# Kernel tuning notes

Measured on AMD Instinct MI355X. Metric: run time of the kernel, lower is better.

Reference implementation:

```python
import jax, jax.numpy as jnp
import numpy as np

N_HEADS = 16
ROPE_BASE = 10000.0


def _rope_tables(T, head_dim, dtype):
    inv_freq = 1.0 / (ROPE_BASE ** (jnp.arange(0, head_dim, 2, dtype=jnp.float32) / head_dim))
    t = jnp.arange(T, dtype=jnp.float32)
    freqs = jnp.outer(t, inv_freq)              # (T, head_dim/2)
    emb = jnp.concatenate([freqs, freqs], -1)   # (T, head_dim)
    return jnp.cos(emb).astype(dtype), jnp.sin(emb).astype(dtype)


def _rotate_half(x):
    x1, x2 = jnp.split(x, 2, axis=-1)
    return jnp.concatenate([-x2, x1], axis=-1)


def setup_inputs() -> dict:
    key = jax.random.key(0)
    k1, k2, k3 = jax.random.split(key, 3)
    B, T, C = 2, 2048, 2048
    x = jax.random.normal(k1, (B, T, C), dtype=jnp.float32)
    Wqkv = jax.random.normal(k2, (C, 3 * C), dtype=jnp.float32) * (1.0 / np.sqrt(C))
    Wproj = jax.random.normal(k3, (C, C), dtype=jnp.float32) * (1.0 / np.sqrt(C))
    return {"x": x, "Wqkv": Wqkv, "Wproj": Wproj}


def reference(x, Wqkv, Wproj):
    B, T, C = x.shape
    H = N_HEADS
    D = C // H
    qkv = jnp.einsum('btc,cd->btd', x, Wqkv)            # (B,T,3C)
    q, k, v = jnp.split(qkv, 3, axis=-1)
    # (B,T,C) -> (B,H,T,D)
    q = q.reshape(B, T, H, D).transpose(0, 2, 1, 3)
    k = k.reshape(B, T, H, D).transpose(0, 2, 1, 3)
    v = v.reshape(B, T, H, D).transpose(0, 2, 1, 3)
    cos, sin = _rope_tables(T, D, x.dtype)              # (T,D) each
    q = q * cos + _rotate_half(q) * sin
    k = k * cos + _rotate_half(k) * sin
    scale = 1.0 / jnp.sqrt(jnp.asarray(D, x.dtype))
    att = jnp.einsum('bhqd,bhkd->bhqk', q, k) * scale   # (B,H,T,T)
    causal = jnp.tril(jnp.ones((T, T), dtype=bool))
    att = jnp.where(causal, att, jnp.asarray(-jnp.inf, att.dtype))
    att = jax.nn.softmax(att, axis=-1)
    y = jnp.einsum('bhqk,bhkd->bhqd', att, v)           # (B,H,T,D)
    y = y.transpose(0, 2, 1, 3).reshape(B, T, C)
    return jnp.einsum('btc,cd->btd', y, Wproj)
```

## Files before the change

kernel.cpp:

```cpp
#include <hip/hip_runtime.h>
#include <stdint.h>

#define T_SEQ 2048
#define NH 16
#define HD 128
#define CC 2048
#define N3 6144
#define MM 4096

typedef short bf16x8 __attribute__((ext_vector_type(8)));
typedef float f32x4 __attribute__((ext_vector_type(4)));

__device__ __forceinline__ unsigned short f2bf(float f) {
  unsigned int u = __float_as_uint(f);
  u += 0x7FFF + ((u >> 16) & 1);
  return (unsigned short)(u >> 16);
}
__device__ __forceinline__ float bf2f(unsigned short h) {
  return __uint_as_float(((unsigned int)h) << 16);
}

__global__ __launch_bounds__(256) void k_transpose_cvt(const float* __restrict__ in,
                                                       unsigned short* __restrict__ out,
                                                       int K, int N) {
  __shared__ float tile[32][33];
  int k0 = blockIdx.x * 32;
  int n0 = blockIdx.y * 32;
  int tx = threadIdx.x & 31, ty = threadIdx.x >> 5;
  #pragma unroll
  for (int r = ty; r < 32; r += 8)
    tile[r][tx] = in[(size_t)(k0 + r) * N + n0 + tx];
  __syncthreads();
  #pragma unroll
  for (int r = ty; r < 32; r += 8)
    out[(size_t)(n0 + r) * K + k0 + tx] = f2bf(tile[tx][r]);
}

__global__ __launch_bounds__(256) void k_cvt(const float* __restrict__ in,
                                             unsigned short* __restrict__ out, int n4) {
  int i = blockIdx.x * 256 + threadIdx.x;
  if (i >= n4) return;
  float4 v = ((const float4*)in)[i];
  ushort4 o;
  o.x = f2bf(v.x); o.y = f2bf(v.y); o.z = f2bf(v.z); o.w = f2bf(v.w);
  ((ushort4*)out)[i] = o;
}

template<int NJ, int EPI, int MMAJ>
__global__ __launch_bounds__(512, 1) void k_gemm8(const unsigned short* __restrict__ A,
                                                  const unsigned short* __restrict__ Bt,
                                                  float* __restrict__ C,
                                                  unsigned short* __restrict__ qo,
                                                  unsigned short* __restrict__ ko,
                                                  unsigned short* __restrict__ vo,
                                                  int M, int N, int K) {
  constexpr int BU = NJ / 2;
  constexpr int DSTRIDE = (1 + BU) * 16384;
  extern __shared__ __align__(16) char lds[];
  const int tid = threadIdx.x;
  const int lane = tid & 63;
  const int lr = lane & 15, lg = lane >> 4;
  const int wave = tid >> 6;
  const int wm = wave >> 2, wn = wave & 3;
  const int nwg = gridDim.x;
  const int bid = blockIdx.x;
  const int wg = (bid & 7) * (nwg >> 3) + (bid >> 3);
  const int GX = M >> 7;
  const int GN = N / (NJ * 64);
  const int mt = MMAJ ? (wg % GX) : (wg / GN);
  const int nt = MMAJ ? (wg / GX) : (wg % GN);
  const int m0 = mt * 128, n0 = nt * NJ * 64;
  const int NT = K >> 6;

  auto STAGE = [&](int d, int op, int h, int t) {
    const unsigned short* src = op ? Bt : A;
    const int r0 = (op ? n0 + h * 128 : m0);
    const int kc = t * 64;
    char* base = lds + d * DSTRIDE + op * 16384 + h * 16384;
    #pragma unroll
    for (int l = 0; l < 2; ++l) {
      int p = (l * 512 + tid) * 16;
      int qq = p ^ (((p >> 7) & 7) << 4);
      const unsigned short* g = src + (size_t)(r0 + (qq >> 7)) * K + kc + ((qq & 127) >> 1);
      __builtin_amdgcn_global_load_lds(
          (const __attribute__((address_space(1))) void*)g,
          (__attribute__((address_space(3))) void*)(base + (l * 512 + (tid & 448)) * 16),
          16, 0, 0);
    }
  };
  auto RD = [&](int d, int op, int row, int kb) -> bf16x8 {
    const char* base = lds + d * DSTRIDE + op * 16384;
    int p = row * 128 + kb;
    p ^= ((p >> 7) & 7) << 4;
    return *(const bf16x8*)(base + p);
  };

  f32x4 acc[4][NJ];
  #pragma unroll
  for (int i = 0; i < 4; ++i)
    #pragma unroll
    for (int j = 0; j < NJ; ++j) acc[i][j] = (f32x4){0.f, 0.f, 0.f, 0.f};

  bf16x8 bfrg[NJ][2];

#define PHASE(D, MI, READB, DOST, SD, SO, SH, ST, VM)                                    \
  {                                                                                      \
    if (READB) {                                                                         \
      _Pragma("unroll")                                                                  \
      for (int nj = 0; nj < NJ; ++nj)                                                    \
        _Pragma("unroll")                                                                \
        for (int ks = 0; ks < 2; ++ks)                                                   \
          bfrg[nj][ks] = RD(D, 1, wn * NJ * 16 + nj * 16 + lr, ks * 64 + lg * 16);       \
    }                                                                                    \
    bf16x8 af[2];                                                                        \
    _Pragma("unroll")                                                                    \
    for (int ks = 0; ks < 2; ++ks)                                                       \
      af[ks] = RD(D, 0, wm * 64 + (MI) * 16 + lr, ks * 64 + lg * 16);                    \
    if (DOST) STAGE(SD, SO, SH, ST);                                                     \
    __builtin_amdgcn_s_barrier();                                                        \
    asm volatile("s_waitcnt lgkmcnt(0)" ::: "memory");                                   \
    __builtin_amdgcn_s_setprio(1);                                                       \
    _Pragma("unroll")                                                                    \
    for (int nj = 0; nj < NJ; ++nj)                                                      \
      _Pragma("unroll")                                                                  \
      for (int ks = 0; ks < 2; ++ks)                                                     \
        acc[MI][nj] = __builtin_amdgcn_mfma_f32_16x16x32_bf16(af[ks], bfrg[nj][ks], acc[MI][nj], 0, 0, 0); \
    __builtin_amdgcn_s_setprio(0);                                                       \
    if ((VM) == 6) asm volatile("s_waitcnt vmcnt(6)" ::: "memory");                      \
    if ((VM) == 4) asm volatile("s_waitcnt vmcnt(4)" ::: "memory");                      \
    __builtin_amdgcn_s_barrier();                                                        \
  }

  const int t1 = NT > 1 ? 1 : 0;
  #pragma unroll
  for (int h = 0; h < BU; ++h) STAGE(0, 1, h, 0);
  STAGE(0, 0, 0, 0);
  #pragma unroll
  for (int h = 0; h < BU; ++h) STAGE(1, 1, h, t1);
  if (NJ == 6) asm volatile("s_waitcnt vmcnt(6)" ::: "memory");
  else         asm volatile("s_waitcnt vmcnt(4)" ::: "memory");
  __builtin_amdgcn_s_barrier();

  for (int it = 0; it < (NT >> 1); ++it) {
    const int tb  = 2 * it + 1;
    const int ta1 = min(2 * it + 2, NT - 1);
    const int tb1 = min(2 * it + 3, NT - 1);
    if (NJ == 6) {
      PHASE(0, 0, true,  true, 1, 0, 0, tb,  -1)
      PHASE(0, 1, false, true, 0, 1, 0, ta1, -1)
      PHASE(0, 2, false, true, 0, 1, 1, ta1, -1)
      PHASE(0, 3, false, true, 0, 1, 2, ta1,  6)
      PHASE(1, 0, true,  true, 0, 0, 0, ta1, -1)
      PHASE(1, 1, false, true, 1, 1, 0, tb1, -1)
      PHASE(1, 2, false, true, 1, 1, 1, tb1, -1)
      PHASE(1, 3, false, true, 1, 1, 2, tb1,  6)
    } else {
      PHASE(0, 0, true,  true,  1, 0, 0, tb,  -1)
      PHASE(0, 1, false, true,  0, 1, 0, ta1, -1)
      PHASE(0, 2, false, true,  0, 1, 1, ta1, -1)
      PHASE(0, 3, false, false, 0, 0, 0, 0,    4)
      PHASE(1, 0, true,  true,  0, 0, 0, ta1, -1)
      PHASE(1, 1, false, true,  1, 1, 0, tb1, -1)
      PHASE(1, 2, false, true,  1, 1, 1, tb1, -1)
      PHASE(1, 3, false, false, 0, 0, 0, 0,    4)
    }
  }
#undef PHASE

  #pragma unroll
  for (int mi = 0; mi < 4; ++mi) {
    #pragma unroll
    for (int nj = 0; nj < NJ; ++nj) {
      #pragma unroll
      for (int j = 0; j < 4; ++j) {
        int m = m0 + wm * 64 + mi * 16 + lg * 4 + j;
        int n = n0 + wn * NJ * 16 + nj * 16 + lr;
        float val = acc[mi][nj][j];
        if (EPI == 0) {
          C[(size_t)m * N + n] = val;
        } else {
          int which = n >> 11, cc = n & 2047;
          int h = cc >> 7, d = cc & 127;
          int b = m >> 11, t = m & 2047;
          unsigned short* dst = which == 0 ? qo : (which == 1 ? ko : vo);
          dst[(((size_t)(b * NH + h)) * T_SEQ + t) * HD + d] = f2bf(val);
        }
      }
    }
  }
}

__global__ __launch_bounds__(256) void k_rope(unsigned short* __restrict__ q,
                                              unsigned short* __restrict__ k) {
  int i = blockIdx.x * 256 + threadIdx.x;
  int d = i & 63;
  int t = (i >> 6) & (T_SEQ - 1);
  int bh = i >> 17;
  float invf = exp2f((float)(-2 * d) * (13.287712379549449f / 128.f));
  float ang = (float)t * invf;
  float c = cosf(ang), s = sinf(ang);
  size_t base = ((size_t)bh * T_SEQ + t) * HD + d;
  const float scale = 0.08838834764831845f;
  float q1 = bf2f(q[base]), q2 = bf2f(q[base + 64]);
  q[base]      = f2bf((q1 * c - q2 * s) * scale);
  q[base + 64] = f2bf((q2 * c + q1 * s) * scale);
  float k1 = bf2f(k[base]), k2 = bf2f(k[base + 64]);
  k[base]      = f2bf(k1 * c - k2 * s);
  k[base + 64] = f2bf(k2 * c + k1 * s);
}

__global__ __launch_bounds__(256) void k_transpose_v(const unsigned short* __restrict__ in,
                                                     unsigned short* __restrict__ out) {
  __shared__ unsigned short tile[32][33];
  int bh = blockIdx.z;
  int t0 = blockIdx.x * 32, d0 = blockIdx.y * 32;
  int tx = threadIdx.x & 31, ty = threadIdx.x >> 5;
  const unsigned short* src = in + (size_t)bh * T_SEQ * HD;
  unsigned short* dst = out + (size_t)bh * HD * T_SEQ;
  #pragma unroll
  for (int r = ty; r < 32; r += 8)
    tile[r][tx] = src[(size_t)(t0 + r) * HD + d0 + tx];
  __syncthreads();
  #pragma unroll
  for (int r = ty; r < 32; r += 8)
    dst[(size_t)(d0 + r) * T_SEQ + t0 + tx] = tile[tx][r];
}

__global__ __launch_bounds__(256) void k_attn(const unsigned short* __restrict__ Q,
                                              const unsigned short* __restrict__ K,
                                              const unsigned short* __restrict__ Vt,
                                              unsigned short* __restrict__ Y) {
  __shared__ __align__(16) unsigned short Ks[64 * 128];
  __shared__ __align__(16) unsigned short Vs[128 * 64];
  __shared__ __align__(16) unsigned short Ps[64 * 80];
  const int bh = blockIdx.x;
  const int qt = (T_SEQ / 64 - 1) - blockIdx.y;
  const int b = bh >> 4, h = bh & 15;
  const int tid = threadIdx.x, wave = tid >> 6, lane = tid & 63;
  const int lr = lane & 15, lg = lane >> 4;
  const int q0 = qt * 64;
  const unsigned short* Qb = Q + (size_t)bh * T_SEQ * HD;
  const unsigned short* Kb = K + (size_t)bh * T_SEQ * HD;
  const unsigned short* Vb = Vt + (size_t)bh * HD * T_SEQ;

  int rkA[4], okA[4], rvA[4], ovA[4], bkA[4], bvA[4];
  #pragma unroll
  for (int it = 0; it < 4; ++it) {
    int c = it * 256 + tid;
    rkA[it] = c >> 4; okA[it] = (c & 15) * 8;
    bkA[it] = (rkA[it] * 256 + (c & 15) * 16) ^ ((rkA[it] & 7) << 4);
    rvA[it] = c >> 3; ovA[it] = (c & 7) * 8;
    bvA[it] = (rvA[it] * 128 + (c & 7) * 16) ^ ((rvA[it] & 7) << 4);
  }

  bf16x8 qf[4];
  #pragma unroll
  for (int kk = 0; kk < 4; ++kk)
    qf[kk] = *(const bf16x8*)(Qb + (size_t)(q0 + wave * 16 + lr) * HD + kk * 32 + lg * 8);

  const f32x4 fzero = {0.f, 0.f, 0.f, 0.f};
  f32x4 oacc[8];
  #pragma unroll
  for (int nd = 0; nd < 8; ++nd) oacc[nd] = fzero;
  float mrow[4], lrow[4];
  #pragma unroll
  for (int j = 0; j < 4; ++j) { mrow[j] = -1e30f; lrow[j] = 0.f; }

  bf16x8 kst[4], vst[4];
  #pragma unroll
  for (int it = 0; it < 4; ++it) {
    kst[it] = *(const bf16x8*)(Kb + (size_t)rkA[it] * HD + okA[it]);
    vst[it] = *(const bf16x8*)(Vb + (size_t)rvA[it] * T_SEQ + ovA[it]);
  }

  for (int jt = 0; jt <= qt; ++jt) {
    const int tk0 = jt * 64;
    __syncthreads();
    #pragma unroll
    for (int it = 0; it < 4; ++it) {
      *(bf16x8*)((char*)Ks + bkA[it]) = kst[it];
      *(bf16x8*)((char*)Vs + bvA[it]) = vst[it];
    }
    if (jt < qt) {
      const int nk0 = tk0 + 64;
      #pragma unroll
      for (int it = 0; it < 4; ++it) {
        kst[it] = *(const bf16x8*)(Kb + (size_t)(nk0 + rkA[it]) * HD + okA[it]);
        vst[it] = *(const bf16x8*)(Vb + (size_t)rvA[it] * T_SEQ + nk0 + ovA[it]);
      }
    }
    __syncthreads();

    f32x4 sacc[4];
    #pragma unroll
    for (int nr = 0; nr < 4; ++nr) sacc[nr] = fzero;
    #pragma unroll
    for (int nr = 0; nr < 4; ++nr) {
      #pragma unroll
      for (int kk = 0; kk < 4; ++kk) {
        int row = nr * 16 + lr;
        int byte = (row * 256 + kk * 64 + lg * 16) ^ ((row & 7) << 4);
        bf16x8 kf = *(const bf16x8*)((char*)Ks + byte);
        sacc[nr] = __builtin_amdgcn_mfma_f32_16x16x32_bf16(qf[kk], kf, sacc[nr], 0, 0, 0);
      }
    }

    if (jt == qt) {
      #pragma unroll
      for (int nr = 0; nr < 4; ++nr)
        #pragma unroll
        for (int j = 0; j < 4; ++j) {
          int qg = q0 + wave * 16 + lg * 4 + j;
          int cg = tk0 + nr * 16 + lr;
          if (cg > qg) sacc[nr][j] = -1e30f;
        }
    }

    float oscale[4];
    #pragma unroll
    for (int j = 0; j < 4; ++j) {
      float tmax = fmaxf(fmaxf(sacc[0][j], sacc[1][j]), fmaxf(sacc[2][j], sacc[3][j]));
      #pragma unroll
      for (int m = 1; m <= 8; m <<= 1) tmax = fmaxf(tmax, __shfl_xor(tmax, m));
      float mnew = fmaxf(mrow[j], tmax);
      oscale[j] = __expf(mrow[j] - mnew);
      float rsum = 0.f;
      #pragma unroll
      for (int nr = 0; nr < 4; ++nr) {
        float p = __expf(sacc[nr][j] - mnew);
        Ps[(wave * 16 + lg * 4 + j) * 80 + nr * 16 + lr] = f2bf(p);
        rsum += p;
      }
      #pragma unroll
      for (int m = 1; m <= 8; m <<= 1) rsum += __shfl_xor(rsum, m);
      lrow[j] = lrow[j] * oscale[j] + rsum;
      mrow[j] = mnew;
    }
    #pragma unroll
    for (int nd = 0; nd < 8; ++nd)
      #pragma unroll
      for (int j = 0; j < 4; ++j) oacc[nd][j] *= oscale[j];

    bf16x8 pf[2];
    #pragma unroll
    for (int kk = 0; kk < 2; ++kk)
      pf[kk] = *(const bf16x8*)(Ps + (wave * 16 + lr) * 80 + kk * 32 + lg * 8);
    #pragma unroll
    for (int nd = 0; nd < 8; ++nd) {
      #pragma unroll
      for (int kk = 0; kk < 2; ++kk) {
        int row = nd * 16 + lr;
        int byte = (row * 128 + kk * 64 + lg * 16) ^ ((row & 7) << 4);
        bf16x8 vf = *(const bf16x8*)((char*)Vs + byte);
        oacc[nd] = __builtin_amdgcn_mfma_f32_16x16x32_bf16(pf[kk], vf, oacc[nd], 0, 0, 0);
      }
    }
  }

  #pragma unroll
  for (int j = 0; j < 4; ++j) {
    float inv = 1.f / lrow[j];
    int qg = q0 + wave * 16 + lg * 4 + j;
    size_t base = ((size_t)b * T_SEQ + qg) * CC + h * HD;
    #pragma unroll
    for (int nd = 0; nd < 8; ++nd)
      Y[base + nd * 16 + lr] = f2bf(oacc[nd][j] * inv);
  }
}

extern "C" void kernel_launch(void* const* d_in, const int* in_sizes, int n_in,
                              void* d_out, int out_size, void* d_ws, size_t ws_size,
                              hipStream_t stream) {
  const float* x     = (const float*)d_in[0];
  const float* Wqkv  = (const float*)d_in[1];
  const float* Wproj = (const float*)d_in[2];
  float* out = (float*)d_out;
  char* ws = (char*)d_ws;
  const size_t MB = 1024 * 1024;
  unsigned short* WqkvT  = (unsigned short*)(ws + 0);
  unsigned short* vt     = (unsigned short*)(ws + 0);
  unsigned short* WprojT = (unsigned short*)(ws + 24 * MB);
  unsigned short* xb     = (unsigned short*)(ws + 32 * MB);
  unsigned short* y      = xb;
  unsigned short* q      = (unsigned short*)(ws + 48 * MB);
  unsigned short* k      = (unsigned short*)(ws + 64 * MB);
  unsigned short* v      = (unsigned short*)(ws + 80 * MB);

  k_transpose_cvt<<<dim3(CC / 32, N3 / 32), 256, 0, stream>>>(Wqkv, WqkvT, CC, N3);
  k_transpose_cvt<<<dim3(CC / 32, CC / 32), 256, 0, stream>>>(Wproj, WprojT, CC, CC);
  k_cvt<<<(MM * CC / 4) / 256, 256, 0, stream>>>(x, xb, MM * CC / 4);
  k_gemm8<6, 1, 1><<<dim3((MM / 128) * (N3 / 384)), 512, 131072, stream>>>(
      xb, WqkvT, nullptr, q, k, v, MM, N3, CC);
  k_rope<<<(32 * T_SEQ * 64) / 256, 256, 0, stream>>>(q, k);
  k_transpose_v<<<dim3(T_SEQ / 32, HD / 32, 32), 256, 0, stream>>>(v, vt);
  k_attn<<<dim3(32, T_SEQ / 64), 256, 0, stream>>>(q, k, vt, y);
  k_gemm8<4, 0, 0><<<dim3((MM / 128) * (CC / 256)), 512, 98304, stream>>>(
      y, WprojT, out, nullptr, nullptr, nullptr, MM, CC, CC);
}
```

Measured before the change: 294.1 us.

## Use 256x256 tiles for QKV GEMM with generalized M-tile template

```diff
diff --git a/kernel.cpp b/kernel.cpp
--- a/kernel.cpp
+++ b/kernel.cpp
@@ -46,16 +46,17 @@
   ((ushort4*)out)[i] = o;
 }
 
-template<int NJ, int EPI, int MMAJ>
-__global__ __launch_bounds__(512, 1) void k_gemm8(const unsigned short* __restrict__ A,
+template<int MIW, int NJ, int EPI, int MMAJ>
+__global__ __launch_bounds__(512, 2) void k_gemm8(const unsigned short* __restrict__ A,
                                                   const unsigned short* __restrict__ Bt,
                                                   float* __restrict__ C,
                                                   unsigned short* __restrict__ qo,
                                                   unsigned short* __restrict__ ko,
                                                   unsigned short* __restrict__ vo,
                                                   int M, int N, int K) {
+  constexpr int AU = MIW / 4;
   constexpr int BU = NJ / 2;
-  constexpr int DSTRIDE = (1 + BU) * 16384;
+  constexpr int DSTRIDE = (AU + BU) * 16384;
   extern __shared__ __align__(16) char lds[];
   const int tid = threadIdx.x;
   const int lane = tid & 63;
@@ -65,18 +66,18 @@
   const int nwg = gridDim.x;
   const int bid = blockIdx.x;
   const int wg = (bid & 7) * (nwg >> 3) + (bid >> 3);
-  const int GX = M >> 7;
+  const int GX = M / (MIW * 32);
   const int GN = N / (NJ * 64);
   const int mt = MMAJ ? (wg % GX) : (wg / GN);
   const int nt = MMAJ ? (wg / GX) : (wg % GN);
-  const int m0 = mt * 128, n0 = nt * NJ * 64;
+  const int m0 = mt * MIW * 32, n0 = nt * NJ * 64;
   const int NT = K >> 6;
 
   auto STAGE = [&](int d, int op, int h, int t) {
     const unsigned short* src = op ? Bt : A;
-    const int r0 = (op ? n0 + h * 128 : m0);
+    const int r0 = (op ? n0 : m0) + h * 128;
     const int kc = t * 64;
-    char* base = lds + d * DSTRIDE + op * 16384 + h * 16384;
+    char* base = lds + d * DSTRIDE + op * (AU * 16384) + h * 16384;
     #pragma unroll
     for (int l = 0; l < 2; ++l) {
       int p = (l * 512 + tid) * 16;
@@ -89,21 +90,21 @@
     }
   };
   auto RD = [&](int d, int op, int row, int kb) -> bf16x8 {
-    const char* base = lds + d * DSTRIDE + op * 16384;
+    const char* base = lds + d * DSTRIDE + op * (AU * 16384);
     int p = row * 128 + kb;
     p ^= ((p >> 7) & 7) << 4;
     return *(const bf16x8*)(base + p);
   };
 
-  f32x4 acc[4][NJ];
-  #pragma unroll
-  for (int i = 0; i < 4; ++i)
+  f32x4 acc[MIW][NJ];
+  #pragma unroll
+  for (int i = 0; i < MIW; ++i)
     #pragma unroll
     for (int j = 0; j < NJ; ++j) acc[i][j] = (f32x4){0.f, 0.f, 0.f, 0.f};
 
   bf16x8 bfrg[NJ][2];
 
-#define PHASE(D, MI, READB, DOST, SD, SO, SH, ST, VM)                                    \
+#define PHASE(D, MIB, NMI, READB, DOST, SD, SO, SH, ST, VM)                              \
   {                                                                                      \
     if (READB) {                                                                         \
       _Pragma("unroll")                                                                  \
@@ -112,68 +113,74 @@
         for (int ks = 0; ks < 2; ++ks)                                                   \
           bfrg[nj][ks] = RD(D, 1, wn * NJ * 16 + nj * 16 + lr, ks * 64 + lg * 16);       \
     }                                                                                    \
-    bf16x8 af[2];                                                                        \
+    bf16x8 af[NMI][2];                                                                   \
     _Pragma("unroll")                                                                    \
-    for (int ks = 0; ks < 2; ++ks)                                                       \
-      af[ks] = RD(D, 0, wm * 64 + (MI) * 16 + lr, ks * 64 + lg * 16);                    \
+    for (int mm = 0; mm < NMI; ++mm)                                                     \
+      _Pragma("unroll")                                                                  \
+      for (int ks = 0; ks < 2; ++ks)                                                     \
+        af[mm][ks] = RD(D, 0, wm * MIW * 16 + (MIB + mm) * 16 + lr, ks * 64 + lg * 16);  \
     if (DOST) STAGE(SD, SO, SH, ST);                                                     \
     __builtin_amdgcn_s_barrier();                                                        \
     asm volatile("s_waitcnt lgkmcnt(0)" ::: "memory");                                   \
     __builtin_amdgcn_s_setprio(1);                                                       \
     _Pragma("unroll")                                                                    \
-    for (int nj = 0; nj < NJ; ++nj)                                                      \
+    for (int mm = 0; mm < NMI; ++mm)                                                     \
       _Pragma("unroll")                                                                  \
-      for (int ks = 0; ks < 2; ++ks)                                                     \
-        acc[MI][nj] = __builtin_amdgcn_mfma_f32_16x16x32_bf16(af[ks], bfrg[nj][ks], acc[MI][nj], 0, 0, 0); \
+      for (int nj = 0; nj < NJ; ++nj)                                                    \
+        _Pragma("unroll")                                                                \
+        for (int ks = 0; ks < 2; ++ks)                                                   \
+          acc[MIB + mm][nj] = __builtin_amdgcn_mfma_f32_16x16x32_bf16(af[mm][ks], bfrg[nj][ks], acc[MIB + mm][nj], 0, 0, 0); \
     __builtin_amdgcn_s_setprio(0);                                                       \
-    if ((VM) == 6) asm volatile("s_waitcnt vmcnt(6)" ::: "memory");                      \
     if ((VM) == 4) asm volatile("s_waitcnt vmcnt(4)" ::: "memory");                      \
     __builtin_amdgcn_s_barrier();                                                        \
   }
 
   const int t1 = NT > 1 ? 1 : 0;
-  #pragma unroll
-  for (int h = 0; h < BU; ++h) STAGE(0, 1, h, 0);
-  STAGE(0, 0, 0, 0);
-  #pragma unroll
-  for (int h = 0; h < BU; ++h) STAGE(1, 1, h, t1);
-  if (NJ == 6) asm volatile("s_waitcnt vmcnt(6)" ::: "memory");
-  else         asm volatile("s_waitcnt vmcnt(4)" ::: "memory");
-  __builtin_amdgcn_s_barrier();
+  if constexpr (MIW == 8) {
+    STAGE(0, 1, 0, 0); STAGE(0, 1, 1, 0); STAGE(0, 0, 0, 0); STAGE(0, 0, 1, 0);
+    STAGE(1, 1, 0, t1); STAGE(1, 1, 1, t1);
+    asm volatile("s_waitcnt vmcnt(4)" ::: "memory");
+    __builtin_amdgcn_s_barrier();
+  } else {
+    STAGE(0, 1, 0, 0); STAGE(0, 1, 1, 0); STAGE(0, 0, 0, 0);
+    STAGE(1, 1, 0, t1); STAGE(1, 1, 1, t1);
+    asm volatile("s_waitcnt vmcnt(4)" ::: "memory");
+    __builtin_amdgcn_s_barrier();
+  }
 
   for (int it = 0; it < (NT >> 1); ++it) {
     const int tb  = 2 * it + 1;
     const int ta1 = min(2 * it + 2, NT - 1);
     const int tb1 = min(2 * it + 3, NT - 1);
-    if (NJ == 6) {
-      PHASE(0, 0, true,  true, 1, 0, 0, tb,  -1)
-      PHASE(0, 1, false, true, 0, 1, 0, ta1, -1)
-      PHASE(0, 2, false, true, 0, 1, 1, ta1, -1)
-      PHASE(0, 3, false, true, 0, 1, 2, ta1,  6)
-      PHASE(1, 0, true,  true, 0, 0, 0, ta1, -1)
-      PHASE(1, 1, false, true, 1, 1, 0, tb1, -1)
-      PHASE(1, 2, false, true, 1, 1, 1, tb1, -1)
-      PHASE(1, 3, false, true, 1, 1, 2, tb1,  6)
+    if constexpr (MIW == 8) {
+      PHASE(0, 0, 2, true,  true, 1, 0, 0, tb,  -1)
+      PHASE(0, 2, 2, false, true, 1, 0, 1, tb,  -1)
+      PHASE(0, 4, 2, false, true, 0, 1, 0, ta1, -1)
+      PHASE(0, 6, 2, false, true, 0, 1, 1, ta1,  4)
+      PHASE(1, 0, 2, true,  true, 0, 0, 0, ta1, -1)
+      PHASE(1, 2, 2, false, true, 0, 0, 1, ta1, -1)
+      PHASE(1, 4, 2, false, true, 1, 1, 0, tb1, -1)
+      PHASE(1, 6, 2, false, true, 1, 1, 1, tb1,  4)
     } else {
-      PHASE(0, 0, true,  true,  1, 0, 0, tb,  -1)
-      PHASE(0, 1, false, true,  0, 1, 0, ta1, -1)
-      PHASE(0, 2, false, true,  0, 1, 1, ta1, -1)
-      PHASE(0, 3, false, false, 0, 0, 0, 0,    4)
-      PHASE(1, 0, true,  true,  0, 0, 0, ta1, -1)
-      PHASE(1, 1, false, true,  1, 1, 0, tb1, -1)
-      PHASE(1, 2, false, true,  1, 1, 1, tb1, -1)
-      PHASE(1, 3, false, false, 0, 0, 0, 0,    4)
+      PHASE(0, 0, 1, true,  true,  1, 0, 0, tb,  -1)
+      PHASE(0, 1, 1, false, true,  0, 1, 0, ta1, -1)
+      PHASE(0, 2, 1, false, true,  0, 1, 1, ta1, -1)
+      PHASE(0, 3, 1, false, false, 0, 0, 0, 0,    4)
+      PHASE(1, 0, 1, true,  true,  0, 0, 0, ta1, -1)
+      PHASE(1, 1, 1, false, true,  1, 1, 0, tb1, -1)
+      PHASE(1, 2, 1, false, true,  1, 1, 1, tb1, -1)
+      PHASE(1, 3, 1, false, false, 0, 0, 0, 0,    4)
     }
   }
 #undef PHASE
 
   #pragma unroll
-  for (int mi = 0; mi < 4; ++mi) {
+  for (int mi = 0; mi < MIW; ++mi) {
     #pragma unroll
     for (int nj = 0; nj < NJ; ++nj) {
       #pragma unroll
       for (int j = 0; j < 4; ++j) {
-        int m = m0 + wm * 64 + mi * 16 + lg * 4 + j;
+        int m = m0 + wm * MIW * 16 + mi * 16 + lg * 4 + j;
         int n = n0 + wn * NJ * 16 + nj * 16 + lr;
         float val = acc[mi][nj][j];
         if (EPI == 0) {
@@ -389,11 +396,11 @@
   k_transpose_cvt<<<dim3(CC / 32, N3 / 32), 256, 0, stream>>>(Wqkv, WqkvT, CC, N3);
   k_transpose_cvt<<<dim3(CC / 32, CC / 32), 256, 0, stream>>>(Wproj, WprojT, CC, CC);
   k_cvt<<<(MM * CC / 4) / 256, 256, 0, stream>>>(x, xb, MM * CC / 4);
-  k_gemm8<6, 1, 1><<<dim3((MM / 128) * (N3 / 384)), 512, 131072, stream>>>(
+  k_gemm8<8, 4, 1, 1><<<dim3((MM / 256) * (N3 / 256)), 512, 131072, stream>>>(
       xb, WqkvT, nullptr, q, k, v, MM, N3, CC);
   k_rope<<<(32 * T_SEQ * 64) / 256, 256, 0, stream>>>(q, k);
   k_transpose_v<<<dim3(T_SEQ / 32, HD / 32, 32), 256, 0, stream>>>(v, vt);
   k_attn<<<dim3(32, T_SEQ / 64), 256, 0, stream>>>(q, k, vt, y);
-  k_gemm8<4, 0, 0><<<dim3((MM / 128) * (CC / 256)), 512, 98304, stream>>>(
+  k_gemm8<4, 4, 0, 0><<<dim3((MM / 128) * (CC / 256)), 512, 98304, stream>>>(
       y, WprojT, out, nullptr, nullptr, nullptr, MM, CC, CC);
 }
```

Result: no change. 299.2 us (+1.8%).

## Load K/V fragments directly from global memory into registers in attention kernel

Applied to the files above, without the earlier changes.

```diff
diff --git a/kernel.cpp b/kernel.cpp
--- a/kernel.cpp
+++ b/kernel.cpp
@@ -226,12 +226,10 @@
     dst[(size_t)(d0 + r) * T_SEQ + t0 + tx] = tile[tx][r];
 }
 
-__global__ __launch_bounds__(256) void k_attn(const unsigned short* __restrict__ Q,
-                                              const unsigned short* __restrict__ K,
-                                              const unsigned short* __restrict__ Vt,
-                                              unsigned short* __restrict__ Y) {
-  __shared__ __align__(16) unsigned short Ks[64 * 128];
-  __shared__ __align__(16) unsigned short Vs[128 * 64];
+__global__ __launch_bounds__(256, 2) void k_attn(const unsigned short* __restrict__ Q,
+                                                 const unsigned short* __restrict__ K,
+                                                 const unsigned short* __restrict__ Vt,
+                                                 unsigned short* __restrict__ Y) {
   __shared__ __align__(16) unsigned short Ps[64 * 80];
   const int bh = blockIdx.x;
   const int qt = (T_SEQ / 64 - 1) - blockIdx.y;
@@ -243,16 +241,6 @@
   const unsigned short* Kb = K + (size_t)bh * T_SEQ * HD;
   const unsigned short* Vb = Vt + (size_t)bh * HD * T_SEQ;
 
-  int rkA[4], okA[4], rvA[4], ovA[4], bkA[4], bvA[4];
-  #pragma unroll
-  for (int it = 0; it < 4; ++it) {
-    int c = it * 256 + tid;
-    rkA[it] = c >> 4; okA[it] = (c & 15) * 8;
-    bkA[it] = (rkA[it] * 256 + (c & 15) * 16) ^ ((rkA[it] & 7) << 4);
-    rvA[it] = c >> 3; ovA[it] = (c & 7) * 8;
-    bvA[it] = (rvA[it] * 128 + (c & 7) * 16) ^ ((rvA[it] & 7) << 4);
-  }
-
   bf16x8 qf[4];
   #pragma unroll
   for (int kk = 0; kk < 4; ++kk)
@@ -266,44 +254,33 @@
   #pragma unroll
   for (int j = 0; j < 4; ++j) { mrow[j] = -1e30f; lrow[j] = 0.f; }
 
-  bf16x8 kst[4], vst[4];
-  #pragma unroll
-  for (int it = 0; it < 4; ++it) {
-    kst[it] = *(const bf16x8*)(Kb + (size_t)rkA[it] * HD + okA[it]);
-    vst[it] = *(const bf16x8*)(Vb + (size_t)rvA[it] * T_SEQ + ovA[it]);
-  }
-
   for (int jt = 0; jt <= qt; ++jt) {
     const int tk0 = jt * 64;
-    __syncthreads();
-    #pragma unroll
-    for (int it = 0; it < 4; ++it) {
-      *(bf16x8*)((char*)Ks + bkA[it]) = kst[it];
-      *(bf16x8*)((char*)Vs + bvA[it]) = vst[it];
-    }
-    if (jt < qt) {
-      const int nk0 = tk0 + 64;
-      #pragma unroll
-      for (int it = 0; it < 4; ++it) {
-        kst[it] = *(const bf16x8*)(Kb + (size_t)(nk0 + rkA[it]) * HD + okA[it]);
-        vst[it] = *(const bf16x8*)(Vb + (size_t)rvA[it] * T_SEQ + nk0 + ovA[it]);
-      }
-    }
-    __syncthreads();
+
+    bf16x8 kf[4][4];
+    #pragma unroll
+    for (int nr = 0; nr < 4; ++nr)
+      #pragma unroll
+      for (int kk = 0; kk < 4; ++kk)
+        kf[nr][kk] = *(const bf16x8*)(Kb + (size_t)(tk0 + nr * 16 + lr) * HD + kk * 32 + lg * 8);
 
     f32x4 sacc[4];
     #pragma unroll
     for (int nr = 0; nr < 4; ++nr) sacc[nr] = fzero;
-    #pragma unroll
-    for (int nr = 0; nr < 4; ++nr) {
-      #pragma unroll
-      for (int kk = 0; kk < 4; ++kk) {
-        int row = nr * 16 + lr;
-        int byte = (row * 256 + kk * 64 + lg * 16) ^ ((row & 7) << 4);
-        bf16x8 kf = *(const bf16x8*)((char*)Ks + byte);
-        sacc[nr] = __builtin_amdgcn_mfma_f32_16x16x32_bf16(qf[kk], kf, sacc[nr], 0, 0, 0);
-      }
-    }
+    __builtin_amdgcn_s_setprio(1);
+    #pragma unroll
+    for (int nr = 0; nr < 4; ++nr)
+      #pragma unroll
+      for (int kk = 0; kk < 4; ++kk)
+        sacc[nr] = __builtin_amdgcn_mfma_f32_16x16x32_bf16(qf[kk], kf[nr][kk], sacc[nr], 0, 0, 0);
+    __builtin_amdgcn_s_setprio(0);
+
+    bf16x8 vf[8][2];
+    #pragma unroll
+    for (int nd = 0; nd < 8; ++nd)
+      #pragma unroll
+      for (int kk = 0; kk < 2; ++kk)
+        vf[nd][kk] = *(const bf16x8*)(Vb + (size_t)(nd * 16 + lr) * T_SEQ + tk0 + kk * 32 + lg * 8);
 
     if (jt == qt) {
       #pragma unroll
@@ -345,16 +322,13 @@
     #pragma unroll
     for (int kk = 0; kk < 2; ++kk)
       pf[kk] = *(const bf16x8*)(Ps + (wave * 16 + lr) * 80 + kk * 32 + lg * 8);
-    #pragma unroll
-    for (int nd = 0; nd < 8; ++nd) {
-      #pragma unroll
-      for (int kk = 0; kk < 2; ++kk) {
-        int row = nd * 16 + lr;
-        int byte = (row * 128 + kk * 64 + lg * 16) ^ ((row & 7) << 4);
-        bf16x8 vf = *(const bf16x8*)((char*)Vs + byte);
-        oacc[nd] = __builtin_amdgcn_mfma_f32_16x16x32_bf16(pf[kk], vf, oacc[nd], 0, 0, 0);
-      }
-    }
+    __builtin_amdgcn_s_setprio(1);
+    #pragma unroll
+    for (int nd = 0; nd < 8; ++nd)
+      #pragma unroll
+      for (int kk = 0; kk < 2; ++kk)
+        oacc[nd] = __builtin_amdgcn_mfma_f32_16x16x32_bf16(pf[kk], vf[nd][kk], oacc[nd], 0, 0, 0);
+    __builtin_amdgcn_s_setprio(0);
   }
 
   #pragma unroll
```

After: 451.1 us. +53.4%, slower.
